# Kernel tuning notes

Measured on AMD Instinct MI355X. Metric: run time of the kernel, lower is better.

Reference implementation:

```python
import jax, jax.numpy as jnp
import numpy as np

N_NODES = 100000


def gcn_conv(x, W, b, src, dst, n_nodes):
    """PyG-style GCNConv: h = D^{-1/2} (A + I) D^{-1/2} (x @ W) + b.

    src/dst already include self-loops. Symmetric normalization with
    degrees computed on the destination index (in-degree incl. self-loop).
    """
    h = x @ W  # [N, out] - transform before propagate (cheap gather dim)
    deg = jax.ops.segment_sum(jnp.ones_like(dst, dtype=h.dtype), dst,
                              num_segments=n_nodes)  # [N]
    dinv = jnp.where(deg > 0, jax.lax.rsqrt(deg), 0.0)  # deg^{-1/2}, 0 for isolated
    norm = dinv[src] * dinv[dst]  # [E]
    msg = h[src] * norm[:, None]  # gather + normalize, [E, out]
    out = jax.ops.segment_sum(msg, dst, num_segments=n_nodes)  # scatter-sum
    return out + b


def setup_inputs() -> dict:
    key = jax.random.key(0)
    k1, k2, k3, k4 = jax.random.split(key, 4)
    in_dim, hidden, n_edges = 128, 32, 3200000
    x = jax.random.normal(k1, (N_NODES, in_dim), dtype=jnp.float32)
    edge_index = jax.random.randint(k2, (2, n_edges), 0, N_NODES, dtype=jnp.int64)
    W1 = jax.random.normal(k3, (in_dim, hidden), dtype=jnp.float32) / np.sqrt(in_dim)
    b1 = jnp.zeros((hidden,), dtype=jnp.float32)
    W2 = jax.random.normal(k4, (hidden, 1), dtype=jnp.float32) / np.sqrt(hidden)
    b2 = jnp.zeros((1,), dtype=jnp.float32)
    return {"x": x, "edge_index": edge_index, "W1": W1, "b1": b1,
            "W2": W2, "b2": b2}


def reference(x, edge_index, W1, b1, W2, b2):
    n = x.shape[0]
    loops = jnp.arange(n, dtype=edge_index.dtype)
    src = jnp.concatenate([edge_index[0], loops])  # add self-loops
    dst = jnp.concatenate([edge_index[1], loops])
    h = jax.nn.relu(gcn_conv(x, W1, b1, src, dst, n))
    out = jax.nn.sigmoid(gcn_conv(h, W2, b2, src, dst, n))
    return out.squeeze(-1)  # [N]
```

## Files before the change

kernel.cpp:

```cpp
#include <hip/hip_runtime.h>
#include <hip/hip_bf16.h>
#include <stdint.h>

#define IN_DIM 128
#define HID 32
#define CSHIFT 7
#define CNODES 128
#define NPART 8
#define SUBCAP 672
#define TILE 4096
#define NBC_MAX 800

#define FPS1 524288.0f
#define IFPS1 (1.0f / 524288.0f)
#define FPS2 262144.0f
#define IFPS2 (1.0f / 262144.0f)

__device__ __forceinline__ float bf_lo(uint u) {
    uint t = u << 16; return *(float*)&t;
}
__device__ __forceinline__ float bf_hi(uint u) {
    uint t = u & 0xFFFF0000u; return *(float*)&t;
}

__global__ __launch_bounds__(256) void binB_kernel(const int* __restrict__ src,
                                                   const int* __restrict__ dst,
                                                   int* __restrict__ pcursor,
                                                   int* __restrict__ pbuf,
                                                   int e, int nbc) {
    __shared__ int hist[NBC_MAX];
    __shared__ int gbase[NBC_MAX];
    int part = blockIdx.x & (NPART - 1);
    int base = blockIdx.x * TILE;
    int cnt = min(TILE, e - base);
    if (cnt <= 0) return;
    for (int i = threadIdx.x; i < nbc; i += 256) hist[i] = 0;
    __syncthreads();
    for (int i = threadIdx.x; i < cnt; i += 256) {
        int d = dst[base + i];
        atomicAdd(&hist[d >> CSHIFT], 1);
    }
    __syncthreads();
    for (int i = threadIdx.x; i < nbc; i += 256) {
        int c = hist[i];
        gbase[i] = (c > 0) ? atomicAdd(&pcursor[part * nbc + i], c) : 0;
        hist[i] = 0;
    }
    __syncthreads();
    for (int i = threadIdx.x; i < cnt; i += 256) {
        int s = src[base + i];
        int d = dst[base + i];
        int bin = d >> CSHIFT;
        int slot = atomicAdd(&hist[bin], 1);
        int pos = gbase[bin] + slot;
        if (pos < SUBCAP)
            pbuf[(size_t)(part * nbc + bin) * SUBCAP + pos] = s | ((d & (CNODES - 1)) << 17);
    }
}

__global__ __launch_bounds__(256) void deg_kernel(const int* __restrict__ pcursor,
                                                  const int* __restrict__ pbuf,
                                                  float* __restrict__ dinv_g,
                                                  int n, int nbc) {
    int b = blockIdx.x;
    __shared__ int hist[CNODES];
    int tid = threadIdx.x;
    int w = tid >> 6, lane = tid & 63;
    if (tid < CNODES) hist[tid] = 0;
    __syncthreads();
#pragma unroll
    for (int pp = 0; pp < 2; pp++) {
        int p = w + pp * 4;
        int cnt = min(pcursor[p * nbc + b], SUBCAP);
        const int* seg = pbuf + (size_t)(p * nbc + b) * SUBCAP;
        for (int i = lane; i < cnt; i += 64)
            atomicAdd(&hist[__builtin_nontemporal_load(seg + i) >> 17], 1);
    }
    __syncthreads();
    if (tid < CNODES) {
        int node = b * CNODES + tid;
        if (node < n) dinv_g[node] = rsqrtf((float)hist[tid] + 1.0f);
    }
}

__global__ __launch_bounds__(256) void mm1_kernel(const float* __restrict__ dinv,
                                                  const float* __restrict__ x,
                                                  const float* __restrict__ W1,
                                                  __hip_bfloat16* __restrict__ h1s,
                                                  int n) {
    int b = blockIdx.x;
    __shared__ float Ws[IN_DIM * 36];
    __shared__ float xs[CNODES * 36];
    int tid = threadIdx.x;
    for (int i = tid; i < IN_DIM * HID; i += 256)
        Ws[(i >> 5) * 36 + (i & 31)] = W1[i];
    int gj = tid & 7;
    int gn = tid >> 3;
    float acc[4][4];
#pragma unroll
    for (int i = 0; i < 4; i++)
#pragma unroll
        for (int j = 0; j < 4; j++) acc[i][j] = 0.f;
    for (int kc = 0; kc < 4; kc++) {
        __syncthreads();
#pragma unroll
        for (int t = 0; t < 4; t++) {
            int f4id = tid + 256 * t;
            int row = f4id >> 3, c4 = f4id & 7;
            int node = b * CNODES + row;
            float4 xv = make_float4(0.f, 0.f, 0.f, 0.f);
            if (node < n)
                xv = *(const float4*)(x + (size_t)node * IN_DIM + kc * 32 + c4 * 4);
            *(float4*)(xs + row * 36 + c4 * 4) = xv;
        }
        __syncthreads();
#pragma unroll
        for (int k4 = 0; k4 < 8; k4++) {
            int kb = kc * 32 + k4 * 4;
            float4 wf0 = *(const float4*)(Ws + (kb + 0) * 36 + gj * 4);
            float4 wf1 = *(const float4*)(Ws + (kb + 1) * 36 + gj * 4);
            float4 wf2 = *(const float4*)(Ws + (kb + 2) * 36 + gj * 4);
            float4 wf3 = *(const float4*)(Ws + (kb + 3) * 36 + gj * 4);
#pragma unroll
            for (int i = 0; i < 4; i++) {
                float4 xv = *(const float4*)(xs + (gn + 32 * i) * 36 + k4 * 4);
                acc[i][0] += xv.x * wf0.x + xv.y * wf1.x + xv.z * wf2.x + xv.w * wf3.x;
                acc[i][1] += xv.x * wf0.y + xv.y * wf1.y + xv.z * wf2.y + xv.w * wf3.y;
                acc[i][2] += xv.x * wf0.z + xv.y * wf1.z + xv.z * wf2.z + xv.w * wf3.z;
                acc[i][3] += xv.x * wf0.w + xv.y * wf1.w + xv.z * wf2.w + xv.w * wf3.w;
            }
        }
    }
#pragma unroll
    for (int i = 0; i < 4; i++) {
        int node = b * CNODES + gn + 32 * i;
        if (node < n) {
            float dv = dinv[node];
            __hip_bfloat162 p0 = __float22bfloat162_rn(
                make_float2(acc[i][0] * dv, acc[i][1] * dv));
            __hip_bfloat162 p1 = __float22bfloat162_rn(
                make_float2(acc[i][2] * dv, acc[i][3] * dv));
            uint2 u;
            u.x = *(uint*)&p0;
            u.y = *(uint*)&p1;
            *(uint2*)(h1s + (size_t)node * HID + gj * 4) = u;
        }
    }
}

__global__ __launch_bounds__(512) void agg1_kernel(const int* __restrict__ pcursor,
                                                   const int* __restrict__ pbuf,
                                                   const float* __restrict__ dinv,
                                                   const __hip_bfloat16* __restrict__ h1s,
                                                   const float* __restrict__ b1,
                                                   const float* __restrict__ W2,
                                                   float* __restrict__ h2s, int n, int nbc) {
    int b = blockIdx.x;
    __shared__ int acc[CNODES * 33];
    __shared__ int ls[NPART * SUBCAP];
    int tid = threadIdx.x;
    const uint* h1u = (const uint*)h1s;
    {
        int row = tid >> 4, u = tid & 15;
        for (int rr = row; rr < CNODES; rr += 32) {
            int node = b * CNODES + rr;
            uint uv = (node < n) ? h1u[(size_t)node * 16 + u] : 0u;
            acc[rr * 33 + 2 * u]     = __float2int_rn(bf_lo(uv) * FPS1);
            acc[rr * 33 + 2 * u + 1] = __float2int_rn(bf_hi(uv) * FPS1);
        }
    }
    int w = tid >> 6;
    int lane = tid & 63;
    int cnt = min(pcursor[w * nbc + b], SUBCAP);
    const int* seg = pbuf + (size_t)(w * nbc + b) * SUBCAP;
    int* lw = ls + w * SUBCAP;
    for (int i = lane; i < cnt; i += 64)
        lw[i] = __builtin_nontemporal_load(seg + i);
    __syncthreads();
    int g = lane >> 4, j2 = lane & 15;
    int nmain = cnt & ~15;
    for (int i0 = 0; i0 < nmain; i0 += 16) {
        int4 v = *(const int4*)(lw + i0 + 4 * g);
        uint uA = h1u[(size_t)(v.x & 0x1FFFF) * 16 + j2];
        uint uB = h1u[(size_t)(v.y & 0x1FFFF) * 16 + j2];
        uint uC = h1u[(size_t)(v.z & 0x1FFFF) * 16 + j2];
        uint uD = h1u[(size_t)(v.w & 0x1FFFF) * 16 + j2];
        atomicAdd(&acc[(v.x >> 17) * 33 + 2 * j2],     __float2int_rn(bf_lo(uA) * FPS1));
        atomicAdd(&acc[(v.x >> 17) * 33 + 2 * j2 + 1], __float2int_rn(bf_hi(uA) * FPS1));
        atomicAdd(&acc[(v.y >> 17) * 33 + 2 * j2],     __float2int_rn(bf_lo(uB) * FPS1));
        atomicAdd(&acc[(v.y >> 17) * 33 + 2 * j2 + 1], __float2int_rn(bf_hi(uB) * FPS1));
        atomicAdd(&acc[(v.z >> 17) * 33 + 2 * j2],     __float2int_rn(bf_lo(uC) * FPS1));
        atomicAdd(&acc[(v.z >> 17) * 33 + 2 * j2 + 1], __float2int_rn(bf_hi(uC) * FPS1));
        atomicAdd(&acc[(v.w >> 17) * 33 + 2 * j2],     __float2int_rn(bf_lo(uD) * FPS1));
        atomicAdd(&acc[(v.w >> 17) * 33 + 2 * j2 + 1], __float2int_rn(bf_hi(uD) * FPS1));
    }
    for (int i = nmain + g; i < cnt; i += 4) {
        int v = lw[i];
        uint uu = h1u[(size_t)(v & 0x1FFFF) * 16 + j2];
        atomicAdd(&acc[(v >> 17) * 33 + 2 * j2],     __float2int_rn(bf_lo(uu) * FPS1));
        atomicAdd(&acc[(v >> 17) * 33 + 2 * j2 + 1], __float2int_rn(bf_hi(uu) * FPS1));
    }
    __syncthreads();
    int node_l = tid >> 2, jp = tid & 3;
    int node = b * CNODES + node_l;
    if (node < n) {
        float dd = dinv[node];
        float pv = 0.f;
#pragma unroll
        for (int q = 0; q < 8; q++) {
            int j = jp * 8 + q;
            float v = (float)acc[node_l * 33 + j] * IFPS1 * dd + b1[j];
            v = fmaxf(v, 0.f);
            pv += v * W2[j];
        }
        pv += __shfl_xor(pv, 1);
        pv += __shfl_xor(pv, 2);
        if (jp == 0) h2s[node] = pv * dd;
    }
}

__global__ __launch_bounds__(512) void agg2_kernel(const int* __restrict__ pcursor,
                                                   const int* __restrict__ pbuf,
                                                   const float* __restrict__ dinv,
                                                   const float* __restrict__ h2s,
                                                   const float* __restrict__ b2,
                                                   float* __restrict__ out, int n, int nbc) {
    int b = blockIdx.x;
    __shared__ int acc2[CNODES];
    int tid = threadIdx.x;
    if (tid < CNODES) acc2[tid] = 0;
    __syncthreads();
    int w = tid >> 6;
    int lane = tid & 63;
    int cnt = min(pcursor[w * nbc + b], SUBCAP);
    const int* seg = pbuf + (size_t)(w * nbc + b) * SUBCAP;
    for (int i = lane; i < cnt; i += 64) {
        int v = seg[i];
        atomicAdd(&acc2[v >> 17], __float2int_rn(h2s[v & 0x1FFFF] * FPS2));
    }
    __syncthreads();
    if (tid < CNODES) {
        int node = b * CNODES + tid;
        if (node < n) {
            float val = ((float)acc2[tid] * IFPS2 + h2s[node]) * dinv[node] + b2[0];
            out[node] = 1.f / (1.f + expf(-val));
        }
    }
}

extern "C" void kernel_launch(void* const* d_in, const int* in_sizes, int n_in,
                              void* d_out, int out_size, void* d_ws, size_t ws_size,
                              hipStream_t stream) {
    const float* x  = (const float*)d_in[0];
    const int*   ei = (const int*)d_in[1];
    const float* W1 = (const float*)d_in[2];
    const float* b1 = (const float*)d_in[3];
    const float* W2 = (const float*)d_in[4];
    const float* b2 = (const float*)d_in[5];
    float* out = (float*)d_out;

    const int n = in_sizes[0] / IN_DIM;
    const int e = in_sizes[1] / 2;
    const int* src = ei;
    const int* dst = ei + e;
    const int nbc = (n + CNODES - 1) >> CSHIFT;

    int* pbuf = (int*)d_ws;
    __hip_bfloat16* h1s = (__hip_bfloat16*)(pbuf + (size_t)NPART * nbc * SUBCAP);
    float* dinv    = (float*)(h1s + (size_t)n * HID);
    float* h2s     = dinv + n;
    int*   pcursor = (int*)(h2s + n);

    const int B = 256;
    int gBin = (e + TILE - 1) / TILE;
    int m  = NPART * nbc;

    hipMemsetAsync(pcursor, 0, (size_t)m * sizeof(int), stream);
    binB_kernel<<<gBin, B, 0, stream>>>(src, dst, pcursor, pbuf, e, nbc);
    deg_kernel<<<nbc, B, 0, stream>>>(pcursor, pbuf, dinv, n, nbc);
    mm1_kernel<<<nbc, B, 0, stream>>>(dinv, x, W1, h1s, n);
    agg1_kernel<<<nbc, 512, 0, stream>>>(pcursor, pbuf, dinv, h1s, b1, W2, h2s, n, nbc);
    agg2_kernel<<<nbc, 512, 0, stream>>>(pcursor, pbuf, dinv, h2s, b2, out, n, nbc);
}
```

Baseline: 234.8 us.

## Fuse degree counting into the x@W1 kernel and prefetch x chunks through registers

Merges the degree-histogram kernel into the first matrix-multiply kernel. Each wave's bucket reads and shared-memory atomics are interleaved across the four K-chunks of the GEMM, and dinv is computed in-block rather than re-read from global memory. The next x chunk is now prefetched into registers while the current chunk is being computed. The binning kernel also loads its 16 src/dst pairs per thread into registers once instead of reading dst twice. This removes a launch and a pass over global memory, at the cost of more register pressure and a more complex synchronisation schedule.

```diff
diff --git a/kernel.cpp b/kernel.cpp
--- a/kernel.cpp
+++ b/kernel.cpp
@@ -34,86 +34,102 @@
     int base = blockIdx.x * TILE;
     int cnt = min(TILE, e - base);
     if (cnt <= 0) return;
-    for (int i = threadIdx.x; i < nbc; i += 256) hist[i] = 0;
-    __syncthreads();
-    for (int i = threadIdx.x; i < cnt; i += 256) {
-        int d = dst[base + i];
-        atomicAdd(&hist[d >> CSHIFT], 1);
-    }
-    __syncthreads();
-    for (int i = threadIdx.x; i < nbc; i += 256) {
+    int tid = threadIdx.x;
+    for (int i = tid; i < nbc; i += 256) hist[i] = 0;
+    int s[16], d[16];
+#pragma unroll
+    for (int j = 0; j < 16; j++) {
+        int i = tid + 256 * j;
+        bool m = i < cnt;
+        d[j] = m ? dst[base + i] : -1;
+        s[j] = m ? src[base + i] : 0;
+    }
+    __syncthreads();
+#pragma unroll
+    for (int j = 0; j < 16; j++)
+        if (d[j] >= 0) atomicAdd(&hist[d[j] >> CSHIFT], 1);
+    __syncthreads();
+    for (int i = tid; i < nbc; i += 256) {
         int c = hist[i];
         gbase[i] = (c > 0) ? atomicAdd(&pcursor[part * nbc + i], c) : 0;
         hist[i] = 0;
     }
     __syncthreads();
-    for (int i = threadIdx.x; i < cnt; i += 256) {
-        int s = src[base + i];
-        int d = dst[base + i];
-        int bin = d >> CSHIFT;
+#pragma unroll
+    for (int j = 0; j < 16; j++) {
+        if (d[j] < 0) continue;
+        int bin = d[j] >> CSHIFT;
         int slot = atomicAdd(&hist[bin], 1);
         int pos = gbase[bin] + slot;
         if (pos < SUBCAP)
-            pbuf[(size_t)(part * nbc + bin) * SUBCAP + pos] = s | ((d & (CNODES - 1)) << 17);
-    }
-}
-
-__global__ __launch_bounds__(256) void deg_kernel(const int* __restrict__ pcursor,
-                                                  const int* __restrict__ pbuf,
-                                                  float* __restrict__ dinv_g,
-                                                  int n, int nbc) {
+            pbuf[(size_t)(part * nbc + bin) * SUBCAP + pos] = s[j] | ((d[j] & (CNODES - 1)) << 17);
+    }
+}
+
+__global__ __launch_bounds__(256) void degmm_kernel(const int* __restrict__ pcursor,
+                                                    const int* __restrict__ pbuf,
+                                                    float* __restrict__ dinv_g,
+                                                    const float* __restrict__ x,
+                                                    const float* __restrict__ W1,
+                                                    __hip_bfloat16* __restrict__ h1s,
+                                                    int n, int nbc) {
     int b = blockIdx.x;
+    __shared__ float Ws[IN_DIM * 36];
+    __shared__ float xs[CNODES * 36];
     __shared__ int hist[CNODES];
     int tid = threadIdx.x;
     int w = tid >> 6, lane = tid & 63;
     if (tid < CNODES) hist[tid] = 0;
-    __syncthreads();
-#pragma unroll
-    for (int pp = 0; pp < 2; pp++) {
-        int p = w + pp * 4;
-        int cnt = min(pcursor[p * nbc + b], SUBCAP);
-        const int* seg = pbuf + (size_t)(p * nbc + b) * SUBCAP;
-        for (int i = lane; i < cnt; i += 64)
-            atomicAdd(&hist[__builtin_nontemporal_load(seg + i) >> 17], 1);
-    }
-    __syncthreads();
-    if (tid < CNODES) {
-        int node = b * CNODES + tid;
-        if (node < n) dinv_g[node] = rsqrtf((float)hist[tid] + 1.0f);
-    }
-}
-
-__global__ __launch_bounds__(256) void mm1_kernel(const float* __restrict__ dinv,
-                                                  const float* __restrict__ x,
-                                                  const float* __restrict__ W1,
-                                                  __hip_bfloat16* __restrict__ h1s,
-                                                  int n) {
-    int b = blockIdx.x;
-    __shared__ float Ws[IN_DIM * 36];
-    __shared__ float xs[CNODES * 36];
-    int tid = threadIdx.x;
     for (int i = tid; i < IN_DIM * HID; i += 256)
         Ws[(i >> 5) * 36 + (i & 31)] = W1[i];
+    int cntA = min(pcursor[w * nbc + b], SUBCAP);
+    int cntB = min(pcursor[(w + 4) * nbc + b], SUBCAP);
+    const int* segA = pbuf + (size_t)(w * nbc + b) * SUBCAP;
+    const int* segB = pbuf + (size_t)((w + 4) * nbc + b) * SUBCAP;
     int gj = tid & 7;
     int gn = tid >> 3;
+    float4 stg[4];
+#pragma unroll
+    for (int t = 0; t < 4; t++) {
+        int f4id = tid + 256 * t;
+        int row = f4id >> 3, c4 = f4id & 7;
+        int node = b * CNODES + row;
+        stg[t] = (node < n) ? *(const float4*)(x + (size_t)node * IN_DIM + c4 * 4)
+                            : make_float4(0.f, 0.f, 0.f, 0.f);
+    }
+    __syncthreads();
+#pragma unroll
+    for (int t = 0; t < 4; t++) {
+        int f4id = tid + 256 * t;
+        *(float4*)(xs + (f4id >> 3) * 36 + (f4id & 7) * 4) = stg[t];
+    }
+    __syncthreads();
     float acc[4][4];
 #pragma unroll
     for (int i = 0; i < 4; i++)
 #pragma unroll
         for (int j = 0; j < 4; j++) acc[i][j] = 0.f;
     for (int kc = 0; kc < 4; kc++) {
-        __syncthreads();
-#pragma unroll
-        for (int t = 0; t < 4; t++) {
-            int f4id = tid + 256 * t;
-            int row = f4id >> 3, c4 = f4id & 7;
-            int node = b * CNODES + row;
-            float4 xv = make_float4(0.f, 0.f, 0.f, 0.f);
-            if (node < n)
-                xv = *(const float4*)(x + (size_t)node * IN_DIM + kc * 32 + c4 * 4);
-            *(float4*)(xs + row * 36 + c4 * 4) = xv;
-        }
-        __syncthreads();
+        if (kc < 3) {
+#pragma unroll
+            for (int t = 0; t < 4; t++) {
+                int f4id = tid + 256 * t;
+                int row = f4id >> 3, c4 = f4id & 7;
+                int node = b * CNODES + row;
+                stg[t] = (node < n)
+                    ? *(const float4*)(x + (size_t)node * IN_DIM + (kc + 1) * 32 + c4 * 4)
+                    : make_float4(0.f, 0.f, 0.f, 0.f);
+            }
+        }
+        int dv[6];
+#pragma unroll
+        for (int t = 0; t < 6; t++) {
+            int idx = lane + 64 * (kc * 3 + (t % 3));
+            bool useB = (t >= 3);
+            int cc = useB ? cntB : cntA;
+            const int* sp = useB ? segB : segA;
+            dv[t] = (idx < cc) ? __builtin_nontemporal_load(sp + idx) : -1;
+        }
 #pragma unroll
         for (int k4 = 0; k4 < 8; k4++) {
             int kb = kc * 32 + k4 * 4;
@@ -130,12 +146,28 @@
                 acc[i][3] += xv.x * wf0.w + xv.y * wf1.w + xv.z * wf2.w + xv.w * wf3.w;
             }
         }
+#pragma unroll
+        for (int t = 0; t < 6; t++)
+            if (dv[t] >= 0) atomicAdd(&hist[dv[t] >> 17], 1);
+        __syncthreads();
+        if (kc < 3) {
+#pragma unroll
+            for (int t = 0; t < 4; t++) {
+                int f4id = tid + 256 * t;
+                *(float4*)(xs + (f4id >> 3) * 36 + (f4id & 7) * 4) = stg[t];
+            }
+            __syncthreads();
+        }
+    }
+    if (tid < CNODES) {
+        int node = b * CNODES + tid;
+        if (node < n) dinv_g[node] = rsqrtf((float)hist[tid] + 1.0f);
     }
 #pragma unroll
     for (int i = 0; i < 4; i++) {
         int node = b * CNODES + gn + 32 * i;
         if (node < n) {
-            float dv = dinv[node];
+            float dv = rsqrtf((float)hist[gn + 32 * i] + 1.0f);
             __hip_bfloat162 p0 = __float22bfloat162_rn(
                 make_float2(acc[i][0] * dv, acc[i][1] * dv));
             __hip_bfloat162 p1 = __float22bfloat162_rn(
@@ -277,8 +309,7 @@
 
     hipMemsetAsync(pcursor, 0, (size_t)m * sizeof(int), stream);
     binB_kernel<<<gBin, B, 0, stream>>>(src, dst, pcursor, pbuf, e, nbc);
-    deg_kernel<<<nbc, B, 0, stream>>>(pcursor, pbuf, dinv, n, nbc);
-    mm1_kernel<<<nbc, B, 0, stream>>>(dinv, x, W1, h1s, n);
+    degmm_kernel<<<nbc, B, 0, stream>>>(pcursor, pbuf, dinv, x, W1, h1s, n, nbc);
     agg1_kernel<<<nbc, 512, 0, stream>>>(pcursor, pbuf, dinv, h1s, b1, W2, h2s, n, nbc);
     agg2_kernel<<<nbc, 512, 0, stream>>>(pcursor, pbuf, dinv, h2s, b2, out, n, nbc);
 }
```

Result: slower. 587.2 us (+150.1%).

## Fuse degree count into binning and dinv into mm1; halve mm1 tile

Applied to the files above, without the earlier changes.

Removes the separate degree kernel. In-degrees are now accumulated with global atomics inside the binning kernel, and mm1 computes dinv from them and writes it out. The binning kernel now loads its 16 src/dst pairs per thread once into registers instead of reading dst twice. mm1 processes 64 nodes per block instead of 128, which doubles the grid. The cost is 3.2M extra global atomics on scattered addresses and a larger memset.

```diff
diff --git a/kernel.cpp b/kernel.cpp
--- a/kernel.cpp
+++ b/kernel.cpp
@@ -6,6 +6,7 @@
 #define HID 32
 #define CSHIFT 7
 #define CNODES 128
+#define MMNODES 64
 #define NPART 8
 #define SUBCAP 672
 #define TILE 4096
@@ -27,6 +28,7 @@
                                                    const int* __restrict__ dst,
                                                    int* __restrict__ pcursor,
                                                    int* __restrict__ pbuf,
+                                                   int* __restrict__ deg,
                                                    int e, int nbc) {
     __shared__ int hist[NBC_MAX];
     __shared__ int gbase[NBC_MAX];
@@ -34,80 +36,65 @@
     int base = blockIdx.x * TILE;
     int cnt = min(TILE, e - base);
     if (cnt <= 0) return;
-    for (int i = threadIdx.x; i < nbc; i += 256) hist[i] = 0;
-    __syncthreads();
-    for (int i = threadIdx.x; i < cnt; i += 256) {
-        int d = dst[base + i];
-        atomicAdd(&hist[d >> CSHIFT], 1);
-    }
-    __syncthreads();
-    for (int i = threadIdx.x; i < nbc; i += 256) {
+    int tid = threadIdx.x;
+    for (int i = tid; i < nbc; i += 256) hist[i] = 0;
+    int s[16], d[16];
+#pragma unroll
+    for (int j = 0; j < 16; j++) {
+        int i = tid + 256 * j;
+        bool m = i < cnt;
+        d[j] = m ? dst[base + i] : -1;
+        s[j] = m ? src[base + i] : 0;
+    }
+    __syncthreads();
+#pragma unroll
+    for (int j = 0; j < 16; j++)
+        if (d[j] >= 0) atomicAdd(&hist[d[j] >> CSHIFT], 1);
+    __syncthreads();
+    for (int i = tid; i < nbc; i += 256) {
         int c = hist[i];
         gbase[i] = (c > 0) ? atomicAdd(&pcursor[part * nbc + i], c) : 0;
         hist[i] = 0;
     }
     __syncthreads();
-    for (int i = threadIdx.x; i < cnt; i += 256) {
-        int s = src[base + i];
-        int d = dst[base + i];
-        int bin = d >> CSHIFT;
+#pragma unroll
+    for (int j = 0; j < 16; j++) {
+        if (d[j] < 0) continue;
+        int bin = d[j] >> CSHIFT;
         int slot = atomicAdd(&hist[bin], 1);
         int pos = gbase[bin] + slot;
         if (pos < SUBCAP)
-            pbuf[(size_t)(part * nbc + bin) * SUBCAP + pos] = s | ((d & (CNODES - 1)) << 17);
-    }
-}
-
-__global__ __launch_bounds__(256) void deg_kernel(const int* __restrict__ pcursor,
-                                                  const int* __restrict__ pbuf,
+            pbuf[(size_t)(part * nbc + bin) * SUBCAP + pos] = s[j] | ((d[j] & (CNODES - 1)) << 17);
+        atomicAdd(&deg[d[j]], 1);
+    }
+}
+
+__global__ __launch_bounds__(256) void mm1_kernel(const int* __restrict__ deg,
                                                   float* __restrict__ dinv_g,
-                                                  int n, int nbc) {
-    int b = blockIdx.x;
-    __shared__ int hist[CNODES];
-    int tid = threadIdx.x;
-    int w = tid >> 6, lane = tid & 63;
-    if (tid < CNODES) hist[tid] = 0;
-    __syncthreads();
-#pragma unroll
-    for (int pp = 0; pp < 2; pp++) {
-        int p = w + pp * 4;
-        int cnt = min(pcursor[p * nbc + b], SUBCAP);
-        const int* seg = pbuf + (size_t)(p * nbc + b) * SUBCAP;
-        for (int i = lane; i < cnt; i += 64)
-            atomicAdd(&hist[__builtin_nontemporal_load(seg + i) >> 17], 1);
-    }
-    __syncthreads();
-    if (tid < CNODES) {
-        int node = b * CNODES + tid;
-        if (node < n) dinv_g[node] = rsqrtf((float)hist[tid] + 1.0f);
-    }
-}
-
-__global__ __launch_bounds__(256) void mm1_kernel(const float* __restrict__ dinv,
                                                   const float* __restrict__ x,
                                                   const float* __restrict__ W1,
                                                   __hip_bfloat16* __restrict__ h1s,
                                                   int n) {
-    int b = blockIdx.x;
+    int base = blockIdx.x * MMNODES;
     __shared__ float Ws[IN_DIM * 36];
-    __shared__ float xs[CNODES * 36];
+    __shared__ float xs[MMNODES * 36];
     int tid = threadIdx.x;
     for (int i = tid; i < IN_DIM * HID; i += 256)
         Ws[(i >> 5) * 36 + (i & 31)] = W1[i];
     int gj = tid & 7;
     int gn = tid >> 3;
-    float acc[4][4];
-#pragma unroll
-    for (int i = 0; i < 4; i++)
+    float acc[2][4];
+#pragma unroll
+    for (int i = 0; i < 2; i++)
 #pragma unroll
         for (int j = 0; j < 4; j++) acc[i][j] = 0.f;
     for (int kc = 0; kc < 4; kc++) {
         __syncthreads();
 #pragma unroll
-        for (int t = 0; t < 4; t++) {
+        for (int t = 0; t < 2; t++) {
             int f4id = tid + 256 * t;
             int row = f4id >> 3, c4 = f4id & 7;
-            int node = b * CNODES + row;
+            int node = base + row;
             float4 xv = make_float4(0.f, 0.f, 0.f, 0.f);
             if (node < n)
                 xv = *(const float4*)(x + (size_t)node * IN_DIM + kc * 32 + c4 * 4);
@@ -122,7 +109,7 @@
             float4 wf2 = *(const float4*)(Ws + (kb + 2) * 36 + gj * 4);
             float4 wf3 = *(const float4*)(Ws + (kb + 3) * 36 + gj * 4);
 #pragma unroll
-            for (int i = 0; i < 4; i++) {
+            for (int i = 0; i < 2; i++) {
                 float4 xv = *(const float4*)(xs + (gn + 32 * i) * 36 + k4 * 4);
                 acc[i][0] += xv.x * wf0.x + xv.y * wf1.x + xv.z * wf2.x + xv.w * wf3.x;
                 acc[i][1] += xv.x * wf0.y + xv.y * wf1.y + xv.z * wf2.y + xv.w * wf3.y;
@@ -132,10 +119,11 @@
         }
     }
 #pragma unroll
-    for (int i = 0; i < 4; i++) {
-        int node = b * CNODES + gn + 32 * i;
+    for (int i = 0; i < 2; i++) {
+        int node = base + gn + 32 * i;
         if (node < n) {
-            float dv = dinv[node];
+            float dv = rsqrtf((float)deg[node] + 1.0f);
+            if (gj == 0) dinv_g[node] = dv;
             __hip_bfloat162 p0 = __float22bfloat162_rn(
                 make_float2(acc[i][0] * dv, acc[i][1] * dv));
             __hip_bfloat162 p1 = __float22bfloat162_rn(
@@ -270,15 +258,16 @@
     float* dinv    = (float*)(h1s + (size_t)n * HID);
     float* h2s     = dinv + n;
     int*   pcursor = (int*)(h2s + n);
+    int*   deg     = pcursor + (size_t)NPART * nbc;
 
     const int B = 256;
     int gBin = (e + TILE - 1) / TILE;
+    int gMM  = (n + MMNODES - 1) / MMNODES;
     int m  = NPART * nbc;
 
-    hipMemsetAsync(pcursor, 0, (size_t)m * sizeof(int), stream);
-    binB_kernel<<<gBin, B, 0, stream>>>(src, dst, pcursor, pbuf, e, nbc);
-    deg_kernel<<<nbc, B, 0, stream>>>(pcursor, pbuf, dinv, n, nbc);
-    mm1_kernel<<<nbc, B, 0, stream>>>(dinv, x, W1, h1s, n);
+    hipMemsetAsync(pcursor, 0, (size_t)(m + n) * sizeof(int), stream);
+    binB_kernel<<<gBin, B, 0, stream>>>(src, dst, pcursor, pbuf, deg, e, nbc);
+    mm1_kernel<<<gMM, B, 0, stream>>>(deg, dinv, x, W1, h1s, n);
     agg1_kernel<<<nbc, 512, 0, stream>>>(pcursor, pbuf, dinv, h1s, b1, W2, h2s, n, nbc);
     agg2_kernel<<<nbc, 512, 0, stream>>>(pcursor, pbuf, dinv, h2s, b2, out, n, nbc);
 }
```

Result: slower. 663.0 us (+182.4%).
